# Optimization experiments

Measured on AMD Instinct MI355X. Metric: run time of the kernel, lower is better.

## Reference

```python
import jax, jax.numpy as jnp
import numpy as np

RX, RY = 10, 10  # box filter half-widths (Angle == 0 path)


def setup_inputs() -> dict:
    key = jax.random.key(0)
    x = jax.random.normal(key, (8, 1, 2048, 2048), dtype=jnp.float32)
    # Angle == 0: constant all-ones box kernel (1,1,2rx+1,2ry+1), a fixed buffer
    kernelx = jnp.ones((1, 1, 2 * RX + 1, 2 * RY + 1), dtype=jnp.float32)
    return {"x": x, "kernelx": kernelx}


def reference(x, kernelx):
    # circular pad: H by rx (top/bottom), W by ry (left/right), matching
    # F.pad(input, (ry, ry, rx, rx), mode='circular')
    xp = jnp.pad(x, ((0, 0), (0, 0), (RX, RX), (RY, RY)), mode="wrap")
    # valid conv with the box kernel -> output has the original HxW
    out = jax.lax.conv_general_dilated(
        xp, kernelx,
        window_strides=(1, 1),
        padding="VALID",
        dimension_numbers=("NCHW", "OIHW", "NCHW"),
    )
    return out
```

## Files before the change

kernel.cpp:

```cpp
#include <hip/hip_runtime.h>


#define HH 2048
#define WW 2048
#define RAD 10
#define DIAM 21
#define TH 64
#define TW 64
#define CS_W (TW + 2 * RAD)
#define CS_STRIDE (CS_W + 1)

__global__ __launch_bounds__(256) void box_filter_v2(
    const float* __restrict__ x, float* __restrict__ out) {
  __shared__ float sCS[TH * CS_STRIDE];

  const int n = blockIdx.z;
  const int h0 = blockIdx.y * TH;
  const int w0 = blockIdx.x * TW;
  const float* __restrict__ xp = x + (size_t)n * HH * WW;
  float* __restrict__ op = out + (size_t)n * HH * WW;
  const int tid = threadIdx.x;

  for (int t = tid; t < CS_W * 4; t += 256) {
    int c = t % CS_W;
    int g = t / CS_W;
    int gc = (w0 - RAD + c) & (WW - 1);
    int rbase = h0 + 16 * g - RAD;
    float v[36];
#pragma unroll
    for (int k = 0; k < 36; ++k)
      v[k] = xp[(size_t)((rbase + k) & (HH - 1)) * WW + gc];
    float s = 0.f;
#pragma unroll
    for (int k = 0; k < DIAM; ++k) s += v[k];
    sCS[(16 * g) * CS_STRIDE + c] = s;
#pragma unroll
    for (int i = 1; i < 16; ++i) {
      s += v[i + DIAM - 1] - v[i - 1];
      sCS[(16 * g + i) * CS_STRIDE + c] = s;
    }
  }
  __syncthreads();

  {
    int r = tid >> 2;
    int cg = tid & 3;
    const float* csrow = &sCS[r * CS_STRIDE + cg * 16];
    float w[36];
#pragma unroll
    for (int k = 0; k < 36; ++k) w[k] = csrow[k];
    float o[16];
    float s = 0.f;
#pragma unroll
    for (int k = 0; k < DIAM; ++k) s += w[k];
    o[0] = s;
#pragma unroll
    for (int j = 1; j < 16; ++j) {
      s += w[j + DIAM - 1] - w[j - 1];
      o[j] = s;
    }
    float4* dst = (float4*)&op[(size_t)(h0 + r) * WW + w0 + cg * 16];
#pragma unroll
    for (int q = 0; q < 4; ++q)
      dst[q] = make_float4(o[4 * q], o[4 * q + 1], o[4 * q + 2], o[4 * q + 3]);
  }
}

extern "C" void kernel_launch(void* const* d_in, const int* in_sizes, int n_in,
                              void* d_out, int out_size, void* d_ws, size_t ws_size,
                              hipStream_t stream) {
  const float* x = (const float*)d_in[0];
  float* out = (float*)d_out;
  dim3 grid(WW / TW, HH / TH, 8);
  dim3 block(256);
  hipLaunchKernelGGL(box_filter_v2, grid, block, 0, stream, x, out);
}
```

Measured before the change: 260.6 us.

## Widen tile to 128 columns with full-column vertical sums per thread

```diff
diff --git a/kernel.cpp b/kernel.cpp
--- a/kernel.cpp
+++ b/kernel.cpp
@@ -6,11 +6,12 @@
 #define RAD 10
 #define DIAM 21
 #define TH 64
-#define TW 64
-#define CS_W (TW + 2 * RAD)
-#define CS_STRIDE (CS_W + 1)
+#define TW 128
+#define NCOL (TW + 2 * RAD)
+#define CS_STRIDE (NCOL + 1)
+#define NROWS (TH + 2 * RAD)
 
-__global__ __launch_bounds__(256) void box_filter_v2(
+__global__ __launch_bounds__(256, 4) void box_filter_v3(
     const float* __restrict__ x, float* __restrict__ out) {
   __shared__ float sCS[TH * CS_STRIDE];
 
@@ -21,47 +22,51 @@
   float* __restrict__ op = out + (size_t)n * HH * WW;
   const int tid = threadIdx.x;
 
-  for (int t = tid; t < CS_W * 4; t += 256) {
-    int c = t % CS_W;
-    int g = t / CS_W;
-    int gc = (w0 - RAD + c) & (WW - 1);
-    int rbase = h0 + 16 * g - RAD;
-    float v[36];
+  if (tid < NCOL) {
+    const int gc = (w0 - RAD + tid) & (WW - 1);
+    float v[NROWS];
+    if (h0 >= RAD && h0 + TH - 1 + RAD < HH) {
+      const float* p = xp + (size_t)(h0 - RAD) * WW + gc;
 #pragma unroll
-    for (int k = 0; k < 36; ++k)
-      v[k] = xp[(size_t)((rbase + k) & (HH - 1)) * WW + gc];
+      for (int k = 0; k < NROWS; ++k) v[k] = p[(size_t)k * WW];
+    } else {
+#pragma unroll
+      for (int k = 0; k < NROWS; ++k)
+        v[k] = xp[(size_t)((h0 - RAD + k) & (HH - 1)) * WW + gc];
+    }
+    asm volatile("" ::: "memory");
     float s = 0.f;
 #pragma unroll
     for (int k = 0; k < DIAM; ++k) s += v[k];
-    sCS[(16 * g) * CS_STRIDE + c] = s;
+    sCS[tid] = s;
 #pragma unroll
-    for (int i = 1; i < 16; ++i) {
+    for (int i = 1; i < TH; ++i) {
       s += v[i + DIAM - 1] - v[i - 1];
-      sCS[(16 * g + i) * CS_STRIDE + c] = s;
+      sCS[i * CS_STRIDE + tid] = s;
     }
   }
   __syncthreads();
 
   {
-    int r = tid >> 2;
-    int cg = tid & 3;
-    const float* csrow = &sCS[r * CS_STRIDE + cg * 16];
-    float w[36];
+    const int r = tid & 63;
+    const int cg = tid >> 6;
+    const float* csrow = &sCS[r * CS_STRIDE + cg * 32];
+    float w_[32 + 2 * RAD];
 #pragma unroll
-    for (int k = 0; k < 36; ++k) w[k] = csrow[k];
-    float o[16];
+    for (int k = 0; k < 52; ++k) w_[k] = csrow[k];
     float s = 0.f;
 #pragma unroll
-    for (int k = 0; k < DIAM; ++k) s += w[k];
+    for (int k = 0; k < DIAM; ++k) s += w_[k];
+    float o[32];
     o[0] = s;
 #pragma unroll
-    for (int j = 1; j < 16; ++j) {
-      s += w[j + DIAM - 1] - w[j - 1];
+    for (int j = 1; j < 32; ++j) {
+      s += w_[j + DIAM - 1] - w_[j - 1];
       o[j] = s;
     }
-    float4* dst = (float4*)&op[(size_t)(h0 + r) * WW + w0 + cg * 16];
+    float4* dst = (float4*)&op[(size_t)(h0 + r) * WW + w0 + cg * 32];
 #pragma unroll
-    for (int q = 0; q < 4; ++q)
+    for (int q = 0; q < 8; ++q)
       dst[q] = make_float4(o[4 * q], o[4 * q + 1], o[4 * q + 2], o[4 * q + 3]);
   }
 }
@@ -73,5 +78,5 @@
   float* out = (float*)d_out;
   dim3 grid(WW / TW, HH / TH, 8);
   dim3 block(256);
-  hipLaunchKernelGGL(box_filter_v2, grid, block, 0, stream, x, out);
+  hipLaunchKernelGGL(box_filter_v3, grid, block, 0, stream, x, out);
 }
```

New measurement: 303.4 us. 1.16x slower.
